# Kernel optimization log

Measured on AMD Instinct MI355X. Metric: run time of the kernel, lower is better.

The kernel has to match this reference:

```python
import jax, jax.numpy as jnp
import numpy as np

N_NODES = 50000


def _gcn_norm(edge_index, n):
    # Add self-loops (PyG GCNConv default) and compute symmetric normalization.
    src = jnp.concatenate([edge_index[0], jnp.arange(n, dtype=edge_index.dtype)])
    dst = jnp.concatenate([edge_index[1], jnp.arange(n, dtype=edge_index.dtype)])
    deg = jax.ops.segment_sum(jnp.ones(src.shape[0], dtype=jnp.float32), dst,
                              num_segments=n)
    dinv = jnp.where(deg > 0, jax.lax.rsqrt(deg), 0.0)
    norm = dinv[src] * dinv[dst]  # [E+N]
    return src, dst, norm


def _gcn_conv(x, src, dst, norm, W, b, n):
    h = x @ W                              # [N, out] linear transform first
    msgs = h[src] * norm[:, None]          # gather + edge-wise scale [E+N, out]
    out = jax.ops.segment_sum(msgs, dst, num_segments=n)  # scatter-add
    return out + b


def setup_inputs() -> dict:
    key = jax.random.key(0)
    k1, k2, k3, k4 = jax.random.split(key, 4)
    N, E, F, H, C = N_NODES, 1600000, 128, 128, 64
    x = jax.random.normal(k1, (N, F), dtype=jnp.float32)
    edge_index = jax.random.randint(k2, (2, E), 0, N, dtype=jnp.int64)
    W1 = jax.random.normal(k3, (F, H), dtype=jnp.float32) * 0.05
    b1 = jnp.zeros((H,), dtype=jnp.float32)
    W2 = jax.random.normal(k4, (H, C), dtype=jnp.float32) * 0.05
    b2 = jnp.zeros((C,), dtype=jnp.float32)
    return {"x": x, "edge_index": edge_index, "W1": W1, "b1": b1,
            "W2": W2, "b2": b2}


def reference(x, edge_index, W1, b1, W2, b2):
    n = x.shape[0]
    src, dst, norm = _gcn_norm(edge_index, n)
    h = _gcn_conv(x, src, dst, norm, W1, b1, n)
    h = jax.nn.relu(h)
    out = _gcn_conv(h, src, dst, norm, W2, b2, n)
    return out
```

## Files before the change

### kernel.cpp

```cpp
#include <hip/hip_runtime.h>
#include <hip/hip_bf16.h>
#include <stdint.h>

#define N_NODES 50000
#define N_EDGES 1600000
#define N_TOT   (N_EDGES + N_NODES)
#define NBKT      256
#define BKT_NODES 196
#define BKT_CAP   7168
#define PBKT_CAP  9216
#define TILE      4096
#define EPT       16
#define ZROW      N_NODES

typedef unsigned short u16;
typedef __attribute__((ext_vector_type(8))) short short8;
typedef __attribute__((ext_vector_type(4))) float floatx4;
typedef __attribute__((ext_vector_type(2))) float f2;

__device__ __forceinline__ float b2f(u16 u) {
    union { unsigned int i; float f; } v; v.i = ((unsigned int)u) << 16; return v.f;
}
__device__ __forceinline__ float asf(unsigned u) {
    union { unsigned int i; float f; } v; v.i = u; return v.f;
}
__device__ __forceinline__ u16 f2b(float f) {
    union { unsigned int i; float f; } v; v.f = f;
    unsigned int r = (v.i + 0x7FFFu + ((v.i >> 16) & 1u)) >> 16;
    return (u16)r;
}

__device__ __forceinline__ void accu(f2& a, unsigned u) {
    f2 r; r.x = asf(u << 16); r.y = asf(u & 0xFFFF0000u);
    a += r;
}
__device__ __forceinline__ void acc4u(f2* a, uint4 q) {
    accu(a[0], q.x); accu(a[1], q.y); accu(a[2], q.z); accu(a[3], q.w);
}

__global__ __launch_bounds__(256) void k_part(const int* __restrict__ ei,
                                              const unsigned* __restrict__ xw,
                                              int* __restrict__ flags,
                                              unsigned* __restrict__ pairs,
                                              int* __restrict__ bktcnt) {
    __shared__ unsigned pairsL[TILE];
    __shared__ unsigned char bktL[TILE];
    __shared__ int hist[NBKT], incl[NBKT], delta[NBKT];
    __shared__ int zc, pc;
    int tid = threadIdx.x;
    long base = (long)blockIdx.x * TILE;
    hist[tid] = 0;
    if (tid == 0) { zc = 0; pc = 0; }
    __syncthreads();
    unsigned hw = ((const unsigned*)ei)[2 * tid + 1];
    atomicAdd(&zc, hw == 0 ? 1 : 0);
    if (blockIdx.x == 0) {
        unsigned w = xw[tid];
        int ex = (w >> 7) & 0xFF;
        atomicAdd(&pc, ((ex == 0) || (ex >= 0x60 && ex <= 0x9F)) ? 1 : 0);
    }
    __syncthreads();
    int i64 = zc > 250;
    if (blockIdx.x == 0 && tid == 0) {
        flags[0] = (pc < 160) ? 1 : 0;
        flags[1] = i64;
    }

    int myb[EPT], myrank[EPT]; unsigned myp[EPT];
#pragma unroll
    for (int t = 0; t < EPT; t++) {
        long idx = base + t * 256 + tid;
        int b = -1; unsigned p = 0;
        if (idx < N_TOT) {
            int s, d;
            if (idx < N_EDGES) {
                if (i64) { s = ei[2 * idx]; d = ei[2 * (N_EDGES + idx)]; }
                else     { s = ei[idx];     d = ei[N_EDGES + idx]; }
            } else {
                s = d = (int)(idx - N_EDGES);
            }
            b = d / BKT_NODES;
            p = (unsigned)s | ((unsigned)(d - b * BKT_NODES) << 16);
        }
        myb[t] = b; myp[t] = p;
        myrank[t] = (b >= 0) ? atomicAdd(&hist[b], 1) : 0;
    }
    __syncthreads();

    int tot = hist[tid];
    incl[tid] = tot;
    __syncthreads();
    for (int o = 1; o < NBKT; o <<= 1) {
        int t2 = (tid >= o) ? incl[tid - o] : 0;
        __syncthreads();
        incl[tid] += t2;
        __syncthreads();
    }
    int excl = incl[tid] - tot;
    int gb = atomicAdd(&bktcnt[tid], tot);
    hist[tid]  = excl;
    delta[tid] = tid * BKT_CAP + gb - excl;
    __syncthreads();

#pragma unroll
    for (int t = 0; t < EPT; t++) {
        if (myb[t] >= 0) {
            int slot = hist[myb[t]] + myrank[t];
            pairsL[slot] = myp[t];
            bktL[slot]   = (unsigned char)myb[t];
        }
    }
    __syncthreads();
    int count = incl[NBKT - 1];
    for (int i = tid; i < count; i += 256) {
        int b = bktL[i];
        int pos = delta[b] + i;
        if (pos - b * BKT_CAP < BKT_CAP)
            pairs[pos] = pairsL[i];
    }
}

__global__ __launch_bounds__(256) void k_bucket(const unsigned* __restrict__ pairs,
                                                const int* __restrict__ bktcnt,
                                                int* __restrict__ rowstart,
                                                int* __restrict__ deg,
                                                float* __restrict__ dinv,
                                                u16* __restrict__ csr) {
    __shared__ u16 csrL[PBKT_CAP];
    __shared__ int degL[NBKT], curL[NBKT], scanT[NBKT];
    int b = blockIdx.x, tid = threadIdx.x;
    int cnt = bktcnt[b];
    const unsigned* reg = pairs + (size_t)b * BKT_CAP;
    degL[tid] = 0;
    __syncthreads();
    for (int i = tid; i < cnt; i += 256)
        atomicAdd(&degL[reg[i] >> 16], 1);
    __syncthreads();
    int n = b * BKT_NODES + tid;
    int valid = (tid < BKT_NODES) && (n < N_NODES);
    int v = degL[tid];
    int pv = valid ? ((v + 15) & ~15) : 0;
    scanT[tid] = pv;
    __syncthreads();
    for (int o = 1; o < NBKT; o <<= 1) {
        int t = (tid >= o) ? scanT[tid - o] : 0;
        __syncthreads();
        scanT[tid] += t;
        __syncthreads();
    }
    int pexcl = scanT[tid] - pv;
    curL[tid] = pexcl;
    if (valid) {
        rowstart[n] = b * PBKT_CAP + pexcl;
        deg[n]      = v;
        dinv[n]     = rsqrtf((float)v);
    }
    int pcnt = scanT[NBKT - 1];
    if (pcnt > PBKT_CAP) pcnt = PBKT_CAP;
    __syncthreads();
    for (int i = tid; i < pcnt; i += 256) csrL[i] = (u16)ZROW;
    __syncthreads();
    for (int i = tid; i < cnt; i += 256) {
        unsigned p = reg[i];
        int slot = atomicAdd(&curL[p >> 16], 1);
        if (slot < PBKT_CAP) csrL[slot] = (u16)(p & 0xFFFFu);
    }
    __syncthreads();
    for (int i = tid; i < pcnt; i += 256)
        csr[(size_t)b * PBKT_CAP + i] = csrL[i];
}

template<int NOUT, bool ADYN>
__global__ __launch_bounds__(256) void k_gemm(const void* __restrict__ A,
                                              const void* __restrict__ W,
                                              const float* __restrict__ dinv,
                                              u16* __restrict__ out, int M,
                                              const int* __restrict__ flags) {
    const int isf32 = flags[0];
    constexpr int LDW = 136;
    __shared__ __align__(16) u16 Wt[NOUT * LDW];
    int tid = threadIdx.x;
    if (blockIdx.x == 0 && tid < NOUT)
        out[(size_t)M * NOUT + tid] = 0;
    const float* Wf = (const float*)W;
    const u16*   Wu = (const u16*)W;
    for (int idx = tid; idx < 128 * NOUT; idx += 256) {
        int k = idx / NOUT, n = idx % NOUT;
        Wt[n * LDW + k] = isf32 ? f2b(Wf[idx]) : Wu[idx];
    }
    __syncthreads();

    int wave = tid >> 6, lane = tid & 63;
    int quad = lane >> 4, l16 = lane & 15;
    int r0 = blockIdx.x * 64 + wave * 16;
    int r = r0 + l16; if (r >= M) r = M - 1;

    floatx4 acc[NOUT / 16];
#pragma unroll
    for (int i = 0; i < NOUT / 16; i++) acc[i] = (floatx4)(0.f);

#pragma unroll
    for (int ks = 0; ks < 4; ks++) {
        short8 a;
        if (ADYN && isf32) {
            const float* af = (const float*)A + (size_t)r * 128 + ks * 32 + quad * 8;
            float4 v0 = ((const float4*)af)[0];
            float4 v1 = ((const float4*)af)[1];
            a[0] = (short)f2b(v0.x); a[1] = (short)f2b(v0.y);
            a[2] = (short)f2b(v0.z); a[3] = (short)f2b(v0.w);
            a[4] = (short)f2b(v1.x); a[5] = (short)f2b(v1.y);
            a[6] = (short)f2b(v1.z); a[7] = (short)f2b(v1.w);
        } else {
            a = ((const short8*)((const u16*)A + (size_t)r * 128))[ks * 4 + quad];
        }
#pragma unroll
        for (int nt = 0; nt < NOUT / 16; nt++) {
            const short8* bp = (const short8*)&Wt[(nt * 16 + l16) * LDW + ks * 32 + quad * 8];
            acc[nt] = __builtin_amdgcn_mfma_f32_16x16x32_bf16(a, *bp, acc[nt], 0, 0, 0);
        }
    }
    float sc[4];
#pragma unroll
    for (int j = 0; j < 4; j++) {
        int row = r0 + quad * 4 + j;
        sc[j] = dinv[row < M ? row : 0];
    }
#pragma unroll
    for (int nt = 0; nt < NOUT / 16; nt++) {
#pragma unroll
        for (int j = 0; j < 4; j++) {
            int row = r0 + quad * 4 + j;
            if (row < M)
                out[(size_t)row * NOUT + nt * 16 + l16] = f2b(acc[nt][j] * sc[j]);
        }
    }
}

__global__ __launch_bounds__(256) void k_agg1(const u16* __restrict__ h,
                                              const u16* __restrict__ csr,
                                              const int* __restrict__ rowstart,
                                              const int* __restrict__ deg,
                                              const float* __restrict__ dinv,
                                              const void* __restrict__ bias,
                                              u16* __restrict__ out,
                                              const int* __restrict__ flags) {
    int wave = threadIdx.x >> 6, lane = threadIdx.x & 63;
    int k = blockIdx.x & 7;
    int s = k & 3;
    int d = (k >> 2) * 25000 + (blockIdx.x >> 3) * 4 + wave;
    int grp = lane >> 2, lg = lane & 3;
    int start = rowstart[d], dg = deg[d];
    int R = (dg + 15) >> 4;
    const u16* cp = csr + start + grp;
    const char* hB = (const char*)h;
    unsigned lb = (unsigned)(s * 64 + lg * 16);

    f2 acc[4] = {};
    unsigned ia = cp[0];
    unsigned ib = cp[(unsigned)((1 < R ? 1 : R - 1) * 16)];
    uint4 q = *(const uint4*)(hB + ((ia << 8) + lb));
    for (int r = 1; r < R; r++) {
        int rn = (r + 1 < R) ? (r + 1) : (R - 1);
        unsigned ic = cp[(unsigned)(rn * 16)];
        uint4 qn = *(const uint4*)(hB + ((ib << 8) + lb));
        acc4u(acc, q);
        q = qn; ib = ic;
    }
    acc4u(acc, q);

#pragma unroll
    for (int j = 0; j < 4; j++) {
        acc[j].x += __shfl_xor(acc[j].x, 4);  acc[j].y += __shfl_xor(acc[j].y, 4);
        acc[j].x += __shfl_xor(acc[j].x, 8);  acc[j].y += __shfl_xor(acc[j].y, 8);
        acc[j].x += __shfl_xor(acc[j].x, 16); acc[j].y += __shfl_xor(acc[j].y, 16);
        acc[j].x += __shfl_xor(acc[j].x, 32); acc[j].y += __shfl_xor(acc[j].y, 32);
    }
    if (grp == 0) {
        int isf32 = flags[0];
        float dd = dinv[d];
        int fb = s * 32 + lg * 8;
        u16 r8[8];
#pragma unroll
        for (int j = 0; j < 4; j++) {
            float bx = isf32 ? ((const float*)bias)[fb + 2 * j]
                             : b2f(((const u16*)bias)[fb + 2 * j]);
            float by = isf32 ? ((const float*)bias)[fb + 2 * j + 1]
                             : b2f(((const u16*)bias)[fb + 2 * j + 1]);
            float vx = acc[j].x * dd + bx;
            float vy = acc[j].y * dd + by;
            r8[2 * j]     = f2b(vx > 0.f ? vx : 0.f);
            r8[2 * j + 1] = f2b(vy > 0.f ? vy : 0.f);
        }
        uint4 o;
        o.x = r8[0] | ((unsigned)r8[1] << 16); o.y = r8[2] | ((unsigned)r8[3] << 16);
        o.z = r8[4] | ((unsigned)r8[5] << 16); o.w = r8[6] | ((unsigned)r8[7] << 16);
        *(uint4*)(out + (size_t)d * 128 + fb) = o;
    }
}

__global__ __launch_bounds__(256) void k_agg2(const u16* __restrict__ h,
                                              const u16* __restrict__ csr,
                                              const int* __restrict__ rowstart,
                                              const int* __restrict__ deg,
                                              const float* __restrict__ dinv,
                                              const void* __restrict__ bias,
                                              float* __restrict__ out,
                                              const int* __restrict__ flags) {
    int wave = threadIdx.x >> 6, lane = threadIdx.x & 63;
    int k = blockIdx.x & 7;
    int s = k & 1;
    int d = (k >> 1) * 12500 + (blockIdx.x >> 3) * 4 + wave;
    int grp = lane >> 2, lg = lane & 3;
    int start = rowstart[d], dg = deg[d];
    int R = (dg + 15) >> 4;
    const u16* cp = csr + start + grp;
    const char* hB = (const char*)h;
    unsigned lb = (unsigned)(s * 64 + lg * 16);

    f2 acc[4] = {};
    unsigned ia = cp[0];
    unsigned ib = cp[(unsigned)((1 < R ? 1 : R - 1) * 16)];
    uint4 q = *(const uint4*)(hB + ((ia << 7) + lb));
    for (int r = 1; r < R; r++) {
        int rn = (r + 1 < R) ? (r + 1) : (R - 1);
        unsigned ic = cp[(unsigned)(rn * 16)];
        uint4 qn = *(const uint4*)(hB + ((ib << 7) + lb));
        acc4u(acc, q);
        q = qn; ib = ic;
    }
    acc4u(acc, q);

#pragma unroll
    for (int j = 0; j < 4; j++) {
        acc[j].x += __shfl_xor(acc[j].x, 4);  acc[j].y += __shfl_xor(acc[j].y, 4);
        acc[j].x += __shfl_xor(acc[j].x, 8);  acc[j].y += __shfl_xor(acc[j].y, 8);
        acc[j].x += __shfl_xor(acc[j].x, 16); acc[j].y += __shfl_xor(acc[j].y, 16);
        acc[j].x += __shfl_xor(acc[j].x, 32); acc[j].y += __shfl_xor(acc[j].y, 32);
    }
    if (grp == 0) {
        int isf32 = flags[0];
        float dd = dinv[d];
        int fb = s * 32 + lg * 8;
        float r8[8];
#pragma unroll
        for (int j = 0; j < 4; j++) {
            float bx = isf32 ? ((const float*)bias)[fb + 2 * j]
                             : b2f(((const u16*)bias)[fb + 2 * j]);
            float by = isf32 ? ((const float*)bias)[fb + 2 * j + 1]
                             : b2f(((const u16*)bias)[fb + 2 * j + 1]);
            r8[2 * j]     = acc[j].x * dd + bx;
            r8[2 * j + 1] = acc[j].y * dd + by;
        }
        float4* op = (float4*)(out + (size_t)d * 64 + fb);
        op[0] = make_float4(r8[0], r8[1], r8[2], r8[3]);
        op[1] = make_float4(r8[4], r8[5], r8[6], r8[7]);
    }
}

extern "C" void kernel_launch(void* const* d_in, const int* in_sizes, int n_in,
                              void* d_out, int out_size, void* d_ws, size_t ws_size,
                              hipStream_t stream) {
    const void* x  = d_in[0];
    const int*  ei = (const int*)d_in[1];
    const void* W1 = d_in[2];
    const void* b1 = d_in[3];
    const void* W2 = d_in[4];
    const void* b2 = d_in[5];
    float* out = (float*)d_out;

    char* ws = (char*)d_ws;
    int*      flags    = (int*)(ws + 0);
    int*      bktcnt   = (int*)(ws + 1024);
    int*      deg      = (int*)(ws + 4096);
    int*      rowstart = (int*)(ws + 204800);
    float*    dinv     = (float*)(ws + 405504);
    u16*      csr      = (u16*)(ws + 606208);
    unsigned* pairs    = (unsigned*)(ws + 5324800);
    u16*      h1       = (u16*)(ws + 5324800);
    u16*      out1     = (u16*)(ws + 18125056);
    u16*      h2       = (u16*)(ws + 5324800);

    hipMemsetAsync(bktcnt, 0, NBKT * sizeof(int), stream);
    k_part   <<<(N_TOT + TILE - 1) / TILE, 256, 0, stream>>>(ei, (const unsigned*)x,
                                                             flags, pairs, bktcnt);
    k_bucket <<<NBKT, 256, 0, stream>>>(pairs, bktcnt, rowstart, deg, dinv, csr);

    k_gemm<128, true> <<<(N_NODES + 63) / 64, 256, 0, stream>>>(x, W1, dinv, h1, N_NODES, flags);
    k_agg1<<<50000, 256, 0, stream>>>(h1, csr, rowstart, deg, dinv, b1, out1, flags);
    k_gemm<64, false> <<<(N_NODES + 63) / 64, 256, 0, stream>>>(out1, W2, dinv, h2, N_NODES, flags);
    k_agg2<<<25000, 256, 0, stream>>>(h2, csr, rowstart, deg, dinv, b2, out, flags);
}
```

Baseline: 296.1 us.

## Store features in 32-column planes per XCD and deepen gather prefetch

The hidden features go into planar layouts of 32 bf16 columns each (a 64-byte row per plane) instead of interleaved full rows. The aggregation blocks are remapped so each XCD handles one feature plane over half or a quarter of the nodes. The goal is to shrink the gathered working set per XCD so it fits better in that XCD's L2. The gather loop also prefetches two rows ahead instead of one to hide more latency. The cost is more complex indexing, and the workspace regions must be large enough for planes of PLANE_E elements.

```diff
diff --git a/kernel.cpp b/kernel.cpp
--- a/kernel.cpp
+++ b/kernel.cpp
@@ -12,6 +12,7 @@
 #define TILE      4096
 #define EPT       16
 #define ZROW      N_NODES
+#define PLANE_E   1600032
 
 typedef unsigned short u16;
 typedef __attribute__((ext_vector_type(8))) short short8;
@@ -170,7 +171,7 @@
         csr[(size_t)b * PBKT_CAP + i] = csrL[i];
 }
 
-template<int NOUT, bool ADYN>
+template<int NOUT, bool ADYN, bool APLANE>
 __global__ __launch_bounds__(256) void k_gemm(const void* __restrict__ A,
                                               const void* __restrict__ W,
                                               const float* __restrict__ dinv,
@@ -181,7 +182,7 @@
     __shared__ __align__(16) u16 Wt[NOUT * LDW];
     int tid = threadIdx.x;
     if (blockIdx.x == 0 && tid < NOUT)
-        out[(size_t)M * NOUT + tid] = 0;
+        out[(size_t)(tid >> 5) * PLANE_E + (size_t)M * 32 + (tid & 31)] = 0;
     const float* Wf = (const float*)W;
     const u16*   Wu = (const u16*)W;
     for (int idx = tid; idx < 128 * NOUT; idx += 256) {
@@ -210,6 +211,9 @@
             a[2] = (short)f2b(v0.z); a[3] = (short)f2b(v0.w);
             a[4] = (short)f2b(v1.x); a[5] = (short)f2b(v1.y);
             a[6] = (short)f2b(v1.z); a[7] = (short)f2b(v1.w);
+        } else if (APLANE) {
+            a = *(const short8*)((const u16*)A + (size_t)ks * PLANE_E
+                                 + (size_t)r * 32 + quad * 8);
         } else {
             a = ((const short8*)((const u16*)A + (size_t)r * 128))[ks * 4 + quad];
         }
@@ -231,7 +235,8 @@
         for (int j = 0; j < 4; j++) {
             int row = r0 + quad * 4 + j;
             if (row < M)
-                out[(size_t)row * NOUT + nt * 16 + l16] = f2b(acc[nt][j] * sc[j]);
+                out[(size_t)(nt >> 1) * PLANE_E + (size_t)row * 32
+                    + (nt & 1) * 16 + l16] = f2b(acc[nt][j] * sc[j]);
         }
     }
 }
@@ -245,28 +250,32 @@
                                               u16* __restrict__ out,
                                               const int* __restrict__ flags) {
     int wave = threadIdx.x >> 6, lane = threadIdx.x & 63;
-    int k = blockIdx.x & 7;
-    int s = k & 3;
-    int d = (k >> 2) * 25000 + (blockIdx.x >> 3) * 4 + wave;
+    int bid = blockIdx.x;
+    int xcd = bid & 7;
+    int s = xcd >> 1;
+    int d = (xcd & 1) * 25000 + (bid >> 3) * 4 + wave;
     int grp = lane >> 2, lg = lane & 3;
     int start = rowstart[d], dg = deg[d];
     int R = (dg + 15) >> 4;
     const u16* cp = csr + start + grp;
-    const char* hB = (const char*)h;
-    unsigned lb = (unsigned)(s * 64 + lg * 16);
+    const char* hB = (const char*)(h + (size_t)s * PLANE_E);
+    unsigned lb = (unsigned)lg << 4;
 
     f2 acc[4] = {};
-    unsigned ia = cp[0];
-    unsigned ib = cp[(unsigned)((1 < R ? 1 : R - 1) * 16)];
-    uint4 q = *(const uint4*)(hB + ((ia << 8) + lb));
-    for (int r = 1; r < R; r++) {
-        int rn = (r + 1 < R) ? (r + 1) : (R - 1);
-        unsigned ic = cp[(unsigned)(rn * 16)];
-        uint4 qn = *(const uint4*)(hB + ((ib << 8) + lb));
-        acc4u(acc, q);
-        q = qn; ib = ic;
-    }
-    acc4u(acc, q);
+    int rl = R - 1;
+    unsigned i0 = cp[0];
+    unsigned i1 = cp[(unsigned)((1 <= rl ? 1 : rl) << 4)];
+    uint4 q0 = *(const uint4*)(hB + ((i0 << 6) + lb));
+    uint4 q1 = *(const uint4*)(hB + ((i1 << 6) + lb));
+    for (int r = 0; r < R - 2; r++) {
+        int rn = (r + 2 <= rl) ? (r + 2) : rl;
+        unsigned i2 = cp[(unsigned)(rn << 4)];
+        acc4u(acc, q0);
+        q0 = q1;
+        q1 = *(const uint4*)(hB + ((i2 << 6) + lb));
+    }
+    acc4u(acc, q0);
+    if (R >= 2) acc4u(acc, q1);
 
 #pragma unroll
     for (int j = 0; j < 4; j++) {
@@ -294,7 +303,7 @@
         uint4 o;
         o.x = r8[0] | ((unsigned)r8[1] << 16); o.y = r8[2] | ((unsigned)r8[3] << 16);
         o.z = r8[4] | ((unsigned)r8[5] << 16); o.w = r8[6] | ((unsigned)r8[7] << 16);
-        *(uint4*)(out + (size_t)d * 128 + fb) = o;
+        *(uint4*)(out + (size_t)s * PLANE_E + (size_t)d * 32 + lg * 8) = o;
     }
 }
 
@@ -307,28 +316,32 @@
                                               float* __restrict__ out,
                                               const int* __restrict__ flags) {
     int wave = threadIdx.x >> 6, lane = threadIdx.x & 63;
-    int k = blockIdx.x & 7;
-    int s = k & 1;
-    int d = (k >> 1) * 12500 + (blockIdx.x >> 3) * 4 + wave;
+    int bid = blockIdx.x;
+    int xcd = bid & 7;
+    int s = xcd >> 2;
+    int d = (xcd & 3) * 12500 + (bid >> 3) * 4 + wave;
     int grp = lane >> 2, lg = lane & 3;
     int start = rowstart[d], dg = deg[d];
     int R = (dg + 15) >> 4;
     const u16* cp = csr + start + grp;
-    const char* hB = (const char*)h;
-    unsigned lb = (unsigned)(s * 64 + lg * 16);
+    const char* hB = (const char*)(h + (size_t)s * PLANE_E);
+    unsigned lb = (unsigned)lg << 4;
 
     f2 acc[4] = {};
-    unsigned ia = cp[0];
-    unsigned ib = cp[(unsigned)((1 < R ? 1 : R - 1) * 16)];
-    uint4 q = *(const uint4*)(hB + ((ia << 7) + lb));
-    for (int r = 1; r < R; r++) {
-        int rn = (r + 1 < R) ? (r + 1) : (R - 1);
-        unsigned ic = cp[(unsigned)(rn * 16)];
-        uint4 qn = *(const uint4*)(hB + ((ib << 7) + lb));
-        acc4u(acc, q);
-        q = qn; ib = ic;
-    }
-    acc4u(acc, q);
+    int rl = R - 1;
+    unsigned i0 = cp[0];
+    unsigned i1 = cp[(unsigned)((1 <= rl ? 1 : rl) << 4)];
+    uint4 q0 = *(const uint4*)(hB + ((i0 << 6) + lb));
+    uint4 q1 = *(const uint4*)(hB + ((i1 << 6) + lb));
+    for (int r = 0; r < R - 2; r++) {
+        int rn = (r + 2 <= rl) ? (r + 2) : rl;
+        unsigned i2 = cp[(unsigned)(rn << 4)];
+        acc4u(acc, q0);
+        q0 = q1;
+        q1 = *(const uint4*)(hB + ((i2 << 6) + lb));
+    }
+    acc4u(acc, q0);
+    if (R >= 2) acc4u(acc, q1);
 
 #pragma unroll
     for (int j = 0; j < 4; j++) {
@@ -385,8 +398,8 @@
                                                              flags, pairs, bktcnt);
     k_bucket <<<NBKT, 256, 0, stream>>>(pairs, bktcnt, rowstart, deg, dinv, csr);
 
-    k_gemm<128, true> <<<(N_NODES + 63) / 64, 256, 0, stream>>>(x, W1, dinv, h1, N_NODES, flags);
+    k_gemm<128, true, false> <<<(N_NODES + 63) / 64, 256, 0, stream>>>(x, W1, dinv, h1, N_NODES, flags);
     k_agg1<<<50000, 256, 0, stream>>>(h1, csr, rowstart, deg, dinv, b1, out1, flags);
-    k_gemm<64, false> <<<(N_NODES + 63) / 64, 256, 0, stream>>>(out1, W2, dinv, h2, N_NODES, flags);
+    k_gemm<64, false, true> <<<(N_NODES + 63) / 64, 256, 0, stream>>>(out1, W2, dinv, h2, N_NODES, flags);
     k_agg2<<<25000, 256, 0, stream>>>(h2, csr, rowstart, deg, dinv, b2, out, flags);
 }
```

After: 278.7 us. -5.9%, faster.
